# Kernel tuning notes

Hardware: AMD Instinct MI355X
Metric: run time of the kernel (lower is better)

Reference implementation:

```python
import jax, jax.numpy as jnp
import numpy as np

POOL = 7; SR = 2; SCALE = 1.0 / 16
NUM_CLASSES = 21
NMS_THR = 0.5; MIN_SIZE = 1.0; TOPK = 100; SCORE_THR = 0.05
BBOX_CLIP = float(np.log(1000.0 / 16))


def roi_align(feat, rois):
    # feat: [C,H,W]; rois: [P,4] xyxy in image coords. torchvision aligned=True, sampling_ratio=2.
    C, H, W = feat.shape
    S = POOL * SR
    x0r = rois[:, 0] * SCALE - 0.5
    y0r = rois[:, 1] * SCALE - 0.5
    bw = (rois[:, 2] - rois[:, 0]) * SCALE / POOL
    bh = (rois[:, 3] - rois[:, 1]) * SCALE / POOL
    t = (jnp.arange(S, dtype=feat.dtype) + 0.5) / SR  # sample offsets in bin units
    ys = y0r[:, None] + bh[:, None] * t  # [P,S]
    xs = x0r[:, None] + bw[:, None] * t  # [P,S]
    vy = (ys >= -1.0) & (ys <= H)
    vx = (xs >= -1.0) & (xs <= W)
    y = jnp.clip(ys, 0.0, H - 1)
    x = jnp.clip(xs, 0.0, W - 1)
    yl = jnp.floor(y).astype(jnp.int32); xl = jnp.floor(x).astype(jnp.int32)
    yh = jnp.minimum(yl + 1, H - 1);     xh = jnp.minimum(xl + 1, W - 1)
    ly = y - yl; lx = x - xl
    hy = 1.0 - ly; hx = 1.0 - lx

    def g(Yi, Xi):  # -> [C,P,S,S]
        return feat[:, Yi[:, :, None], Xi[:, None, :]]

    val = (g(yl, xl) * (hy[:, :, None] * hx[:, None, :])
         + g(yl, xh) * (hy[:, :, None] * lx[:, None, :])
         + g(yh, xl) * (ly[:, :, None] * hx[:, None, :])
         + g(yh, xh) * (ly[:, :, None] * lx[:, None, :]))
    val = val * (vy[:, :, None] & vx[:, None, :])[None].astype(feat.dtype)
    P = rois.shape[0]
    val = val.reshape(C, P, POOL, SR, POOL, SR).mean(axis=(3, 5))  # avg over 2x2 samples/bin
    return val.transpose(1, 0, 2, 3)  # [P,C,POOL,POOL]


def decode(pred, proposals):
    # pred: [N,K,4] (dx,dy,dw,dh); proposals: [N,4]
    w = proposals[:, 2] - proposals[:, 0]
    h = proposals[:, 3] - proposals[:, 1]
    cx = proposals[:, 0] + 0.5 * w
    cy = proposals[:, 1] + 0.5 * h
    dx, dy = pred[..., 0], pred[..., 1]
    dw = jnp.minimum(pred[..., 2], BBOX_CLIP)
    dh = jnp.minimum(pred[..., 3], BBOX_CLIP)
    pcx = dx * w[:, None] + cx[:, None]
    pcy = dy * h[:, None] + cy[:, None]
    pw = jnp.exp(dw) * w[:, None]
    ph = jnp.exp(dh) * h[:, None]
    return jnp.stack([pcx - 0.5 * pw, pcy - 0.5 * ph, pcx + 0.5 * pw, pcy + 0.5 * ph], axis=-1)


def box_iou(b):
    x1, y1, x2, y2 = b[:, 0], b[:, 1], b[:, 2], b[:, 3]
    area = (x2 - x1) * (y2 - y1)
    iw = jnp.maximum(jnp.minimum(x2[:, None], x2[None, :]) - jnp.maximum(x1[:, None], x1[None, :]), 0.0)
    ih = jnp.maximum(jnp.minimum(y2[:, None], y2[None, :]) - jnp.maximum(y1[:, None], y1[None, :]), 0.0)
    inter = iw * ih
    return inter / (area[:, None] + area[None, :] - inter)


def filter_predictions(boxes, labels, scores):
    # score threshold + min-size + per-class greedy NMS + topK, static shapes (padded to TOPK)
    N = scores.shape[0]
    ws = boxes[:, 2] - boxes[:, 0]
    hs = boxes[:, 3] - boxes[:, 1]
    valid = (scores > SCORE_THR) & (ws >= MIN_SIZE) & (hs >= MIN_SIZE)
    skey = jnp.where(valid, scores, -jnp.inf)
    order = jnp.argsort(-skey)
    b = boxes[order]; s = skey[order]; l = labels[order]; v = valid[order]
    # batched_nms via per-class coordinate offset
    off = jax.lax.stop_gradient(jnp.max(boxes) + 1.0)
    ob = jax.lax.stop_gradient(b) + (l.astype(b.dtype) * off)[:, None]
    iou = box_iou(ob)  # [N,N]
    idx = jnp.arange(N)

    def body(keep, i):
        sup = (iou[i] > NMS_THR) & keep[i] & (idx > i)
        return keep & ~sup, None

    keep, _ = jax.lax.scan(body, v, idx)
    rank = jnp.cumsum(keep) - 1
    final = keep & (rank < TOPK)
    pick = jnp.argsort(jnp.where(final, idx, N))[:TOPK]  # kept indices in score order, padded
    ok = final[pick]
    out_boxes = jnp.where(ok[:, None], b[pick], 0.0)
    out_scores = jnp.where(ok, s[pick], 0.0)
    out_labels = jnp.where(ok, l[pick], -1)
    return out_boxes, out_labels, out_scores


def roi_head_forward(image, feat, proposals, fc6_w, fc6_b, fc7_w, fc7_b, cls_w, cls_b, reg_w, reg_b):
    H_img, W_img = image.shape[-2], image.shape[-1]
    pooled = roi_align(feat[0], proposals)  # [P,C,7,7]
    x = pooled.reshape(pooled.shape[0], -1)
    x = jax.nn.relu(x @ fc6_w.T + fc6_b)
    x = jax.nn.relu(x @ fc7_w.T + fc7_b)
    cls_scores = x @ cls_w.T + cls_b                       # [P,K]
    box_pred = (x @ reg_w.T + reg_b).reshape(-1, NUM_CLASSES, 4)
    boxes = decode(box_pred, proposals)                    # [P,K,4]
    scores = jax.nn.softmax(cls_scores, axis=-1)
    boxes = jnp.stack([boxes[..., 0].clip(0, W_img), boxes[..., 1].clip(0, H_img),
                       boxes[..., 2].clip(0, W_img), boxes[..., 3].clip(0, H_img)], axis=-1)
    labels = jnp.broadcast_to(jnp.arange(NUM_CLASSES), scores.shape)
    boxes = boxes[:, 1:].reshape(-1, 4)
    scores = scores[:, 1:].reshape(-1)
    labels = (labels[:, 1:] - 1).reshape(-1)
    return filter_predictions(boxes, labels, scores)


def setup_inputs() -> dict:
    key = jax.random.key(0)
    ks = jax.random.split(key, 12)
    H_img, W_img = 800, 1072
    P, C = 300, 512
    image = jnp.zeros((1, 3, H_img, W_img), jnp.float32)
    feat = jax.random.normal(ks[0], (1, C, H_img // 16, W_img // 16), jnp.float32)
    cx = jax.random.uniform(ks[1], (P,)) * W_img
    cy = jax.random.uniform(ks[2], (P,)) * H_img
    bw = 20.0 + jax.random.uniform(ks[3], (P,)) * 300.0
    bh = 20.0 + jax.random.uniform(ks[4], (P,)) * 300.0
    proposals = jnp.stack([jnp.clip(cx - bw / 2, 0, W_img), jnp.clip(cy - bh / 2, 0, H_img),
                           jnp.clip(cx + bw / 2, 0, W_img), jnp.clip(cy + bh / 2, 0, H_img)], axis=1)
    fin = C * POOL * POOL  # 25088
    D = 1024
    fc6_w = jax.random.normal(ks[5], (D, fin), jnp.float32) / np.sqrt(fin)
    fc6_b = jnp.zeros((D,), jnp.float32)
    fc7_w = jax.random.normal(ks[6], (D, D), jnp.float32) / np.sqrt(D)
    fc7_b = jnp.zeros((D,), jnp.float32)
    cls_w = jax.random.normal(ks[7], (NUM_CLASSES, D), jnp.float32) / np.sqrt(D)
    cls_b = jnp.zeros((NUM_CLASSES,), jnp.float32)
    reg_w = jax.random.normal(ks[8], (NUM_CLASSES * 4, D), jnp.float32) * 0.001
    reg_b = jnp.zeros((NUM_CLASSES * 4,), jnp.float32)
    return {"image": image, "feat": feat, "proposals": proposals,
            "fc6_w": fc6_w, "fc6_b": fc6_b, "fc7_w": fc7_w, "fc7_b": fc7_b,
            "cls_w": cls_w, "cls_b": cls_b, "reg_w": reg_w, "reg_b": reg_b}


def reference(image, feat, proposals, fc6_w, fc6_b, fc7_w, fc7_b, cls_w, cls_b, reg_w, reg_b):
    return roi_head_forward(image, feat, proposals, fc6_w, fc6_b, fc7_w, fc7_b, cls_w, cls_b, reg_w, reg_b)
```

## Files before the change

### kernel.cpp

```cpp
#include <hip/hip_runtime.h>
#include <hip/hip_bf16.h>
#include <math.h>

#define P_N   300
#define C_N   512
#define H_F   50
#define W_F   67
#define HW_F  3350
#define D_N   1024
#define FIN   25088
#define NCLS  21
#define NCAND 6000
#define W_IMG 1072.0f
#define H_IMG 800.0f
#define BBOX_CLIP_F 4.135166556742356f
#define KS6   42
#define STEPS6_PER_Z 19
#define KS7   16
#define STEPS7_PER_Z 2
#define KSH   16
#define STEPSH_PER_Z 2
#define NHEAD 128
#define NW    96
#define A_SCALE 16.0f
#define B_SCALE 256.0f
#define O_SCALE (1.0f / 4096.0f)

typedef __attribute__((ext_vector_type(8)))  _Float16 half8;
typedef __attribute__((ext_vector_type(16))) float    f32x16;

__device__ __forceinline__ void splitA(float f, _Float16& h, _Float16& l) {
  float fs = f * A_SCALE;
  h = (_Float16)fs;
  l = (_Float16)(fs - (float)h);
}

__global__ __launch_bounds__(256) void transpose_feat(const float* __restrict__ feat,
                                                      float* __restrict__ ft) {
  __shared__ float tile[32][33];
  const int s0 = blockIdx.x * 32, c0 = blockIdx.y * 32;
  const int tx = threadIdx.x, ty = threadIdx.y;
  for (int r = ty; r < 32; r += 8) {
    int c = c0 + r, s = s0 + tx;
    tile[r][tx] = (s < HW_F) ? feat[(size_t)c * HW_F + s] : 0.0f;
  }
  __syncthreads();
  for (int r = ty; r < 32; r += 8) {
    int s = s0 + r, c = c0 + tx;
    if (s < HW_F) ft[(size_t)s * C_N + c] = tile[tx][r];
  }
}

__global__ __launch_bounds__(256) void roi_align_k(const float* __restrict__ ft,
                                                   const float* __restrict__ rois,
                                                   _Float16* __restrict__ Xhi,
                                                   _Float16* __restrict__ Xlo) {
  __shared__ _Float16 hbuf[12544] __attribute__((aligned(16)));
  __shared__ _Float16 lbuf[12544] __attribute__((aligned(16)));
  __shared__ int   g_yl[14], g_yh[14], g_xl[14], g_xh[14];
  __shared__ float g_ly[14], g_hy[14], g_lx[14], g_hx[14];
  __shared__ int   g_vy[14], g_vx[14];

  const int p   = blockIdx.x;
  const int ch  = blockIdx.y;
  const int tid = threadIdx.x;

  if (tid < 14) {
    const float rx0 = rois[p*4+0], ry0 = rois[p*4+1], rx1 = rois[p*4+2], ry1 = rois[p*4+3];
    const float x0r = rx0 * 0.0625f - 0.5f;
    const float y0r = ry0 * 0.0625f - 0.5f;
    const float bw  = (rx1 - rx0) * 0.0625f * (1.0f / 7.0f);
    const float bh  = (ry1 - ry0) * 0.0625f * (1.0f / 7.0f);
    const float t   = ((float)tid + 0.5f) * 0.5f;

    const float ys = y0r + bh * t;
    g_vy[tid] = (ys >= -1.0f) && (ys <= (float)H_F);
    float y = fminf(fmaxf(ys, 0.0f), (float)(H_F - 1));
    int yi = (int)floorf(y);
    g_yl[tid] = yi; g_yh[tid] = min(yi + 1, H_F - 1);
    g_ly[tid] = y - (float)yi; g_hy[tid] = 1.0f - (y - (float)yi);

    const float xs = x0r + bw * t;
    g_vx[tid] = (xs >= -1.0f) && (xs <= (float)W_F);
    float x = fminf(fmaxf(xs, 0.0f), (float)(W_F - 1));
    int xi = (int)floorf(x);
    g_xl[tid] = xi; g_xh[tid] = min(xi + 1, W_F - 1);
    g_lx[tid] = x - (float)xi; g_hx[tid] = 1.0f - (x - (float)xi);
  }
  __syncthreads();

  const int c = ch * 256 + tid;
  for (int cell = 0; cell < 49; ++cell) {
    const int py = cell / 7;
    const int px = cell - py * 7;
    float acc = 0.0f;
#pragma unroll
    for (int sy = 0; sy < 2; ++sy) {
      const int iy = 2 * py + sy;
      if (!g_vy[iy]) continue;
      const float ly = g_ly[iy], hy = g_hy[iy];
      const int ry0i = g_yl[iy] * W_F, ry1i = g_yh[iy] * W_F;
#pragma unroll
      for (int sx = 0; sx < 2; ++sx) {
        const int ix = 2 * px + sx;
        if (!g_vx[ix]) continue;
        const float lx = g_lx[ix], hx = g_hx[ix];
        const float* b00 = ft + (size_t)(ry0i + g_xl[ix]) * C_N;
        const float* b01 = ft + (size_t)(ry0i + g_xh[ix]) * C_N;
        const float* b10 = ft + (size_t)(ry1i + g_xl[ix]) * C_N;
        const float* b11 = ft + (size_t)(ry1i + g_xh[ix]) * C_N;
        acc += (hy*hx)*b00[c] + (hy*lx)*b01[c] + (ly*hx)*b10[c] + (ly*lx)*b11[c];
      }
    }
    _Float16 h, l;
    splitA(acc * 0.25f, h, l);
    hbuf[tid * 49 + cell] = h;
    lbuf[tid * 49 + cell] = l;
  }
  __syncthreads();

  const size_t base = (size_t)p * FIN + (size_t)ch * 12544;
  const uint4* hs = (const uint4*)hbuf;
  const uint4* ls = (const uint4*)lbuf;
  uint4* dh = (uint4*)(Xhi + base);
  uint4* dl = (uint4*)(Xlo + base);
  for (int k = tid; k < 1568; k += 256) { dh[k] = hs[k]; dl[k] = ls[k]; }
}

__device__ __forceinline__ int swz(int slot, int ks) {
  return slot ^ ((slot >> 5) & 1) ^ (((slot >> 3) & 1) << 1) ^ ((ks & 1) << 2);
}

__global__ __launch_bounds__(256, 3) void gemm_f16_3p(
    const _Float16* __restrict__ Ahi, const _Float16* __restrict__ Alo,
    const float* __restrict__ Wt, float* __restrict__ Pt,
    int M, int K, int steps_per_z, int ldc)
{
  __shared__ _Float16 lds[16384];
  const int tid  = threadIdx.x;
  const int lane = tid & 63, wave = tid >> 6;
  const int wm = wave >> 1, wn = wave & 1;

  const int GX = gridDim.x, GY = gridDim.y;
  const int T  = GX * GY * gridDim.z;
  int flat = blockIdx.x + GX * (blockIdx.y + GY * blockIdx.z);
  if ((T & 7) == 0) flat = (flat & 7) * (T >> 3) + (flat >> 3);
  const int bx = flat % GX;
  const int by = (flat / GX) % GY;
  const int bz = flat / (GX * GY);

  const int m0 = bx * 128, n0 = by * 128;
  const int steps_total = K >> 5;
  const int s0 = bz * steps_per_z;
  const int s1 = min(s0 + steps_per_z, steps_total);

  f32x16 acc[2][2];
#pragma unroll
  for (int a = 0; a < 2; ++a)
#pragma unroll
    for (int b = 0; b < 2; ++b)
#pragma unroll
      for (int r = 0; r < 16; ++r) acc[a][b][r] = 0.f;

  const int srow = tid >> 2;
  const int j8   = tid & 3;
  const int ksW  = j8 >> 1, kc8 = j8 & 1;
  const int wslot = swz((kc8 << 5) | (srow & 31), ksW);

  for (int step = s0; step < s1; ++step) {
    const int kb = step << 5;
#pragma unroll
    for (int half = 0; half < 2; ++half) {
      const int row = srow + half * 64;
      const int mf  = row >> 5;
      const int gm  = m0 + row;
      uint4 vh = make_uint4(0,0,0,0), vl = make_uint4(0,0,0,0);
      if (gm < M) {
        vh = *reinterpret_cast<const uint4*>(Ahi + (size_t)gm * K + kb + j8 * 8);
        vl = *reinterpret_cast<const uint4*>(Alo + (size_t)gm * K + kb + j8 * 8);
      }
      const int base = (mf * 2 + ksW) * 512 + wslot * 8;
      *reinterpret_cast<uint4*>(&lds[base])        = vh;
      *reinterpret_cast<uint4*>(&lds[4096 + base]) = vl;
    }
#pragma unroll
    for (int half = 0; half < 2; ++half) {
      const int n = srow + half * 64;
      const float* wp = Wt + (size_t)(n0 + n) * K + kb + j8 * 8;
      const float4 f0 = *reinterpret_cast<const float4*>(wp);
      const float4 f1 = *reinterpret_cast<const float4*>(wp + 4);
      float fv[8] = {f0.x, f0.y, f0.z, f0.w, f1.x, f1.y, f1.z, f1.w};
      union { _Float16 h[8]; uint4 v; } uh, ul;
#pragma unroll
      for (int e = 0; e < 8; ++e) {
        float fs = fv[e] * B_SCALE;
        uh.h[e] = (_Float16)fs;
        ul.h[e] = (_Float16)(fs - (float)uh.h[e]);
      }
      const int nf = n >> 5;
      const int base = 8192 + (nf * 2 + ksW) * 512 + wslot * 8;
      *reinterpret_cast<uint4*>(&lds[base])        = uh.v;
      *reinterpret_cast<uint4*>(&lds[4096 + base]) = ul.v;
    }
    __syncthreads();
#pragma unroll
    for (int ks = 0; ks < 2; ++ks) {
      const int rslot = swz(lane, ks) * 8;
      half8 ah[2], al[2], bh[2], bl[2];
#pragma unroll
      for (int mi = 0; mi < 2; ++mi) {
        const int mf = wm * 2 + mi;
        ah[mi] = *reinterpret_cast<const half8*>(&lds[(mf * 2 + ks) * 512 + rslot]);
        al[mi] = *reinterpret_cast<const half8*>(&lds[4096 + (mf * 2 + ks) * 512 + rslot]);
      }
#pragma unroll
      for (int ni = 0; ni < 2; ++ni) {
        const int nf = wn * 2 + ni;
        bh[ni] = *reinterpret_cast<const half8*>(&lds[8192  + (nf * 2 + ks) * 512 + rslot]);
        bl[ni] = *reinterpret_cast<const half8*>(&lds[12288 + (nf * 2 + ks) * 512 + rslot]);
      }
#pragma unroll
      for (int mi = 0; mi < 2; ++mi)
#pragma unroll
        for (int ni = 0; ni < 2; ++ni) {
          acc[mi][ni] = __builtin_amdgcn_mfma_f32_32x32x16_f16(ah[mi], bh[ni], acc[mi][ni], 0, 0, 0);
          acc[mi][ni] = __builtin_amdgcn_mfma_f32_32x32x16_f16(ah[mi], bl[ni], acc[mi][ni], 0, 0, 0);
          acc[mi][ni] = __builtin_amdgcn_mfma_f32_32x32x16_f16(al[mi], bh[ni], acc[mi][ni], 0, 0, 0);
        }
    }
    __syncthreads();
  }
  const int col = lane & 31, rhi = lane >> 5;
  float* outp = Pt + (size_t)bz * ((size_t)M * ldc);
#pragma unroll
  for (int mi = 0; mi < 2; ++mi)
#pragma unroll
    for (int ni = 0; ni < 2; ++ni) {
      const int n = n0 + (wn * 2 + ni) * 32 + col;
      if (n >= ldc) continue;
#pragma unroll
      for (int r = 0; r < 16; ++r) {
        const int m = m0 + (wm * 2 + mi) * 32 + ((r & 3) + 8 * (r >> 2) + 4 * rhi);
        if (m < M) outp[(size_t)m * ldc + n] = acc[mi][ni][r] * O_SCALE;
      }
    }
}

__global__ __launch_bounds__(256) void reduce_bias(
    const float* __restrict__ Pt, const float* __restrict__ bias,
    float* __restrict__ out_f32, _Float16* __restrict__ out_hi, _Float16* __restrict__ out_lo,
    int MN, int KS, int nmask, int relu)
{
  int i = blockIdx.x * 256 + threadIdx.x;
  if (i >= MN) return;
  float s = 0.0f;
  for (int k = 0; k < KS; ++k) s += Pt[(size_t)k * MN + i];
  s += bias[i & nmask];
  if (relu) s = fmaxf(s, 0.0f);
  if (out_f32) out_f32[i] = s;
  if (out_hi) {
    _Float16 h, l; splitA(s, h, l);
    out_hi[i] = h; out_lo[i] = l;
  }
}

__global__ __launch_bounds__(256) void prep_head(const float* __restrict__ cls_w,
                                                 const float* __restrict__ cls_b,
                                                 const float* __restrict__ reg_w,
                                                 const float* __restrict__ reg_b,
                                                 float* __restrict__ Wpad,
                                                 float* __restrict__ bpad,
                                                 int* __restrict__ vcount) {
  const int row = blockIdx.x;
  const int t = threadIdx.x;
  if (row == 0 && t == 0) *vcount = 0;
  const float* src = (row < NCLS) ? (cls_w + (size_t)row * D_N)
                   : (row < 105)  ? (reg_w + (size_t)(row - NCLS) * D_N) : nullptr;
  float4 v = make_float4(0.f, 0.f, 0.f, 0.f);
  if (src) v = reinterpret_cast<const float4*>(src)[t];
  reinterpret_cast<float4*>(Wpad + (size_t)row * D_N)[t] = v;
  if (t == 0)
    bpad[row] = (row < NCLS) ? cls_b[row] : (row < 105) ? reg_b[row - NCLS] : 0.0f;
}

__global__ __launch_bounds__(64) void decode_kernel(const float* __restrict__ logits,
                                                    const float* __restrict__ props,
                                                    float* __restrict__ cboxes,
                                                    unsigned long long* __restrict__ ckeys,
                                                    int* __restrict__ vcount) {
  const int p = blockIdx.x;
  const int lane = threadIdx.x;
  const float* lg = logits + (size_t)p * NHEAD;

  float s = (lane < NCLS) ? lg[lane] : -__builtin_inff();
  float mx = s;
#pragma unroll
  for (int off = 32; off > 0; off >>= 1) mx = fmaxf(mx, __shfl_xor(mx, off));
  float e = (lane < NCLS) ? expf(s - mx) : 0.0f;
  float sum = e;
#pragma unroll
  for (int off = 32; off > 0; off >>= 1) sum += __shfl_xor(sum, off);
  const float sm = e / sum;

  if (lane >= 1 && lane < NCLS) {
    const int c = lane;
    const float x0 = props[p*4+0], y0 = props[p*4+1], x1 = props[p*4+2], y1 = props[p*4+3];
    const float w = x1 - x0, hh = y1 - y0;
    const float cx = x0 + 0.5f * w, cy = y0 + 0.5f * hh;
    const float dx = lg[NCLS + c*4 + 0];
    const float dy = lg[NCLS + c*4 + 1];
    const float dw = fminf(lg[NCLS + c*4 + 2], BBOX_CLIP_F);
    const float dh = fminf(lg[NCLS + c*4 + 3], BBOX_CLIP_F);
    const float pcx = dx * w + cx, pcy = dy * hh + cy;
    const float pw = expf(dw) * w, ph = expf(dh) * hh;
    float bx0 = pcx - 0.5f * pw, by0 = pcy - 0.5f * ph;
    float bx1 = pcx + 0.5f * pw, by1 = pcy + 0.5f * ph;
    bx0 = fminf(fmaxf(bx0, 0.0f), W_IMG);
    by0 = fminf(fmaxf(by0, 0.0f), H_IMG);
    bx1 = fminf(fmaxf(bx1, 0.0f), W_IMG);
    by1 = fminf(fmaxf(by1, 0.0f), H_IMG);
    const int idx = p * 20 + (c - 1);
    cboxes[idx*4+0] = bx0; cboxes[idx*4+1] = by0;
    cboxes[idx*4+2] = bx1; cboxes[idx*4+3] = by1;
    const bool valid = (sm > 0.05f) && ((bx1 - bx0) >= 1.0f) && ((by1 - by0) >= 1.0f);
    if (valid) {
      int pos = atomicAdd(vcount, 1);
      unsigned u = __float_as_uint(sm);
      ckeys[pos] = ((unsigned long long)(~u) << 32) | (unsigned)idx;
    }
  }
}

__global__ __launch_bounds__(1024) void sort_gather(const unsigned long long* __restrict__ ckeys,
                                                    const int* __restrict__ vcount,
                                                    const float* __restrict__ cboxes,
                                                    float4* __restrict__ sbox,
                                                    float* __restrict__ sscore,
                                                    int* __restrict__ slab) {
  __shared__ unsigned long long keys[8192];
  const int tid = threadIdx.x;
  const int V = *vcount;
  int Npad = 64; while (Npad < V) Npad <<= 1;
  for (int i = tid; i < Npad; i += 1024)
    keys[i] = (i < V) ? ckeys[i] : ~0ULL;
  __syncthreads();
  for (int kk = 2; kk <= Npad; kk <<= 1) {
    for (int j = kk >> 1; j > 0; j >>= 1) {
      for (int i = tid; i < Npad; i += 1024) {
        int ij = i ^ j;
        if (ij > i) {
          unsigned long long a = keys[i], b = keys[ij];
          bool up = ((i & kk) == 0);
          if ((a > b) == up) { keys[i] = b; keys[ij] = a; }
        }
      }
      __syncthreads();
    }
  }
  for (int i = tid; i < V; i += 1024) {
    unsigned long long key = keys[i];
    int idx = (int)(key & 0xffffffffu);
    sbox[i]   = *reinterpret_cast<const float4*>(&cboxes[(size_t)idx * 4]);
    sscore[i] = __uint_as_float(~(unsigned)(key >> 32));
    slab[i]   = idx % 20;
  }
}

__global__ __launch_bounds__(256) void iou_matrix(const float4* __restrict__ sbox,
                                                  const int* __restrict__ slab,
                                                  const int* __restrict__ vcount,
                                                  unsigned long long* __restrict__ mask) {
  const int V = *vcount;
  const int i = blockIdx.x * 4 + (threadIdx.x >> 6);
  const int lane = threadIdx.x & 63;
  if (i >= V) return;
  const float4 bi = sbox[i];
  const int li = slab[i];
  const float ai = (bi.z - bi.x) * (bi.w - bi.y);
  const int nw = (V + 63) >> 6;
  for (int w = 0; w < nw; ++w) {
    const int j = (w << 6) + lane;
    bool sup = false;
    if (j > i && j < V && slab[j] == li) {
      const float4 bj = sbox[j];
      const float iw = fminf(bi.z, bj.z) - fmaxf(bi.x, bj.x);
      const float ih = fminf(bi.w, bj.w) - fmaxf(bi.y, bj.y);
      const float inter = fmaxf(iw, 0.0f) * fmaxf(ih, 0.0f);
      const float aj = (bj.z - bj.x) * (bj.w - bj.y);
      sup = inter / (ai + aj - inter) > 0.5f;
    }
    const unsigned long long m = __ballot(sup);
    if (lane == 0) mask[(size_t)i * NW + w] = m;
  }
}

__device__ __forceinline__ unsigned long long bcast_live(unsigned long long live0,
                                                         unsigned long long live1, int w) {
  union { unsigned long long u; uint2 v; } t;
  t.u = (w < 64) ? live0 : live1;
  const int src = w & 63;
  const unsigned lo = __shfl(t.v.x, src);
  const unsigned hi = __shfl(t.v.y, src);
  return ((unsigned long long)hi << 32) | lo;
}

__global__ __launch_bounds__(64) void nms_scan(const float4* __restrict__ sbox,
                                               const float* __restrict__ sscore,
                                               const int* __restrict__ slab,
                                               const int* __restrict__ vcount,
                                               const unsigned long long* __restrict__ mask,
                                               float* __restrict__ out) {
  const int lane = threadIdx.x;
  const int V = min(*vcount, NCAND);
  const int nw = (V + 63) >> 6;
  unsigned long long live0 = ~0ULL, live1 = ~0ULL;
  int nk = 0;
  for (int w = 0; w < nw && nk < 100; ++w) {
    const int nb = V - (w << 6);
    const unsigned long long vmask = (nb >= 64) ? ~0ULL : ((1ULL << nb) - 1ULL);
    unsigned long long wv = bcast_live(live0, live1, w) & vmask;
    while (wv && nk < 100) {
      const int b = __ffsll((long long)wv) - 1;
      const int i = (w << 6) + b;
      if (lane == 0) {
        const float4 bb = sbox[i];
        out[nk*4+0] = bb.x; out[nk*4+1] = bb.y; out[nk*4+2] = bb.z; out[nk*4+3] = bb.w;
        out[400 + nk] = (float)slab[i];
        out[500 + nk] = sscore[i];
      }
      const unsigned long long* mrow = mask + (size_t)i * NW;
      if (lane < nw) live0 &= ~mrow[lane];
      if (64 + lane < nw) live1 &= ~mrow[64 + lane];
      nk++;
      wv = bcast_live(live0, live1, w) & vmask;
      wv &= (b == 63) ? 0ULL : ~((2ULL << b) - 1ULL);
    }
  }
  for (int r = nk + lane; r < 100; r += 64) {
    out[r*4+0] = 0.0f; out[r*4+1] = 0.0f; out[r*4+2] = 0.0f; out[r*4+3] = 0.0f;
    out[400 + r] = -1.0f;
    out[500 + r] = 0.0f;
  }
}

extern "C" void kernel_launch(void* const* d_in, const int* in_sizes, int n_in,
                              void* d_out, int out_size, void* d_ws, size_t ws_size,
                              hipStream_t stream) {
  const float* feat   = (const float*)d_in[1];
  const float* props  = (const float*)d_in[2];
  const float* fc6_w  = (const float*)d_in[3];
  const float* fc6_b  = (const float*)d_in[4];
  const float* fc7_w  = (const float*)d_in[5];
  const float* fc7_b  = (const float*)d_in[6];
  const float* cls_w  = (const float*)d_in[7];
  const float* cls_b  = (const float*)d_in[8];
  const float* reg_w  = (const float*)d_in[9];
  const float* reg_b  = (const float*)d_in[10];

  char* ws = (char*)d_ws;
  size_t off = 0;
  auto alloc = [&](size_t bytes) -> void* {
    void* p = ws + off;
    off += (bytes + 255) & ~(size_t)255;
    return p;
  };

  _Float16* Xhi  = (_Float16*)alloc((size_t)P_N * FIN * 2);
  _Float16* Xlo  = (_Float16*)alloc((size_t)P_N * FIN * 2);
  float*    Pt   = (float*)alloc((size_t)KS6 * P_N * D_N * 4);
  _Float16* h6hi = (_Float16*)alloc((size_t)P_N * D_N * 2);
  _Float16* h6lo = (_Float16*)alloc((size_t)P_N * D_N * 2);
  _Float16* h7hi = (_Float16*)alloc((size_t)P_N * D_N * 2);
  _Float16* h7lo = (_Float16*)alloc((size_t)P_N * D_N * 2);
  float*    Wpad = (float*)alloc((size_t)NHEAD * D_N * 4);
  float*    bpad = (float*)alloc((size_t)NHEAD * 4);
  float*  logits = (float*)alloc((size_t)P_N * NHEAD * 4);
  float*  cboxes = (float*)alloc((size_t)NCAND * 4 * 4);
  unsigned long long* ckeys = (unsigned long long*)alloc((size_t)NCAND * 8);
  float4*   sbox = (float4*)alloc((size_t)NCAND * 16);
  float*  sscore = (float*)alloc((size_t)NCAND * 4);
  int*      slab = (int*)alloc((size_t)NCAND * 4);
  unsigned long long* supmask = (unsigned long long*)alloc((size_t)NCAND * NW * 8);
  int*    vcount = (int*)alloc(256);
  float* ft = Pt;
  (void)ws_size; (void)in_sizes; (void)n_in; (void)out_size;

  prep_head<<<NHEAD, 256, 0, stream>>>(cls_w, cls_b, reg_w, reg_b, Wpad, bpad, vcount);
  transpose_feat<<<dim3((HW_F + 31) / 32, C_N / 32), dim3(32, 8), 0, stream>>>(feat, ft);
  roi_align_k<<<dim3(P_N, 2), 256, 0, stream>>>(ft, props, Xhi, Xlo);
  gemm_f16_3p<<<dim3(3, 8, KS6), 256, 0, stream>>>(Xhi, Xlo, fc6_w, Pt, P_N, FIN, STEPS6_PER_Z, D_N);
  reduce_bias<<<(P_N * D_N + 255) / 256, 256, 0, stream>>>(
      Pt, fc6_b, nullptr, h6hi, h6lo, P_N * D_N, KS6, D_N - 1, 1);
  gemm_f16_3p<<<dim3(3, 8, KS7), 256, 0, stream>>>(h6hi, h6lo, fc7_w, Pt, P_N, D_N, STEPS7_PER_Z, D_N);
  reduce_bias<<<(P_N * D_N + 255) / 256, 256, 0, stream>>>(
      Pt, fc7_b, nullptr, h7hi, h7lo, P_N * D_N, KS7, D_N - 1, 1);
  gemm_f16_3p<<<dim3(3, 1, KSH), 256, 0, stream>>>(h7hi, h7lo, Wpad, Pt, P_N, D_N, STEPSH_PER_Z, NHEAD);
  reduce_bias<<<(P_N * NHEAD + 255) / 256, 256, 0, stream>>>(
      Pt, bpad, logits, nullptr, nullptr, P_N * NHEAD, KSH, NHEAD - 1, 0);
  decode_kernel<<<P_N, 64, 0, stream>>>(logits, props, cboxes, ckeys, vcount);
  sort_gather<<<1, 1024, 0, stream>>>(ckeys, vcount, cboxes, sbox, sscore, slab);
  iou_matrix<<<(NCAND + 3) / 4, 256, 0, stream>>>(sbox, slab, vcount, supmask);
  nms_scan<<<1, 64, 0, stream>>>(sbox, sscore, slab, vcount, supmask, (float*)d_out);
}
```

Baseline: 343.2 us.

## Register-prefetch next K tile in GEMM, halve fc6 split-K, merge prep kernels

The GEMM main loop now loads the next K-step's A and W tiles into registers before writing the current tile to LDS and computing on it. This overlaps global load latency with the MFMA work. The fc6 split-K factor drops from 42 to 21, which doubles steps per block and halves the partial-sum traffic, but also halves the grid. The head-weight padding kernel is folded into the feature transpose kernel to save one launch. The prefetch costs extra registers, which could hurt occupancy at 3 blocks per CU.

```diff
diff --git a/kernel.cpp b/kernel.cpp
--- a/kernel.cpp
+++ b/kernel.cpp
@@ -14,8 +14,8 @@
 #define W_IMG 1072.0f
 #define H_IMG 800.0f
 #define BBOX_CLIP_F 4.135166556742356f
-#define KS6   42
-#define STEPS6_PER_Z 19
+#define KS6   21
+#define STEPS6_PER_Z 38
 #define KS7   16
 #define STEPS7_PER_Z 2
 #define KSH   16
@@ -25,6 +25,7 @@
 #define A_SCALE 16.0f
 #define B_SCALE 256.0f
 #define O_SCALE (1.0f / 4096.0f)
+#define TBLK  1680
 
 typedef __attribute__((ext_vector_type(8)))  _Float16 half8;
 typedef __attribute__((ext_vector_type(16))) float    f32x16;
@@ -35,19 +36,41 @@
   l = (_Float16)(fs - (float)h);
 }
 
-__global__ __launch_bounds__(256) void transpose_feat(const float* __restrict__ feat,
-                                                      float* __restrict__ ft) {
+__global__ __launch_bounds__(256) void prep_transpose(const float* __restrict__ feat,
+                                                      float* __restrict__ ft,
+                                                      const float* __restrict__ cls_w,
+                                                      const float* __restrict__ cls_b,
+                                                      const float* __restrict__ reg_w,
+                                                      const float* __restrict__ reg_b,
+                                                      float* __restrict__ Wpad,
+                                                      float* __restrict__ bpad,
+                                                      int* __restrict__ vcount) {
   __shared__ float tile[32][33];
-  const int s0 = blockIdx.x * 32, c0 = blockIdx.y * 32;
-  const int tx = threadIdx.x, ty = threadIdx.y;
-  for (int r = ty; r < 32; r += 8) {
-    int c = c0 + r, s = s0 + tx;
-    tile[r][tx] = (s < HW_F) ? feat[(size_t)c * HW_F + s] : 0.0f;
-  }
-  __syncthreads();
-  for (int r = ty; r < 32; r += 8) {
-    int s = s0 + r, c = c0 + tx;
-    if (s < HW_F) ft[(size_t)s * C_N + c] = tile[tx][r];
+  const int bid = blockIdx.x;
+  const int tid = threadIdx.x;
+  if (bid < TBLK) {
+    const int bx = bid % 105, byy = bid / 105;
+    const int s0 = bx * 32, c0 = byy * 32;
+    const int tx = tid & 31, ty = tid >> 5;
+    for (int r = ty; r < 32; r += 8) {
+      int c = c0 + r, s = s0 + tx;
+      tile[r][tx] = (s < HW_F) ? feat[(size_t)c * HW_F + s] : 0.0f;
+    }
+    __syncthreads();
+    for (int r = ty; r < 32; r += 8) {
+      int s = s0 + r, c = c0 + tx;
+      if (s < HW_F) ft[(size_t)s * C_N + c] = tile[tx][r];
+    }
+  } else {
+    const int row = bid - TBLK;
+    if (row == 0 && tid == 0) *vcount = 0;
+    const float* src = (row < NCLS) ? (cls_w + (size_t)row * D_N)
+                     : (row < 105)  ? (reg_w + (size_t)(row - NCLS) * D_N) : nullptr;
+    float4 v = make_float4(0.f, 0.f, 0.f, 0.f);
+    if (src) v = reinterpret_cast<const float4*>(src)[tid];
+    reinterpret_cast<float4*>(Wpad + (size_t)row * D_N)[tid] = v;
+    if (tid == 0)
+      bpad[row] = (row < NCLS) ? cls_b[row] : (row < 105) ? reg_b[row - NCLS] : 0.0f;
   }
 }
 
@@ -131,6 +154,58 @@
   return slot ^ ((slot >> 5) & 1) ^ (((slot >> 3) & 1) << 1) ^ ((ks & 1) << 2);
 }
 
+struct SReg { uint4 ah0, ah1, al0, al1; float4 b00, b01, b10, b11; };
+
+__device__ __forceinline__ void stage_load(SReg& R, const _Float16* __restrict__ Ahi,
+                                           const _Float16* __restrict__ Alo,
+                                           const float* __restrict__ Wt,
+                                           int M, int K, int m0, int n0,
+                                           int srow, int j8, int kb) {
+  const int gm0 = m0 + srow, gm1 = m0 + srow + 64;
+  R.ah0 = make_uint4(0,0,0,0); R.al0 = R.ah0; R.ah1 = R.ah0; R.al1 = R.ah0;
+  if (gm0 < M) {
+    R.ah0 = *reinterpret_cast<const uint4*>(Ahi + (size_t)gm0 * K + kb + j8 * 8);
+    R.al0 = *reinterpret_cast<const uint4*>(Alo + (size_t)gm0 * K + kb + j8 * 8);
+  }
+  if (gm1 < M) {
+    R.ah1 = *reinterpret_cast<const uint4*>(Ahi + (size_t)gm1 * K + kb + j8 * 8);
+    R.al1 = *reinterpret_cast<const uint4*>(Alo + (size_t)gm1 * K + kb + j8 * 8);
+  }
+  const float* wp0 = Wt + (size_t)(n0 + srow) * K + kb + j8 * 8;
+  const float* wp1 = Wt + (size_t)(n0 + srow + 64) * K + kb + j8 * 8;
+  R.b00 = *reinterpret_cast<const float4*>(wp0);
+  R.b01 = *reinterpret_cast<const float4*>(wp0 + 4);
+  R.b10 = *reinterpret_cast<const float4*>(wp1);
+  R.b11 = *reinterpret_cast<const float4*>(wp1 + 4);
+}
+
+__device__ __forceinline__ void stage_write(const SReg& R, _Float16* lds,
+                                            int srow, int ksW, int wslot) {
+  const int mf0 = srow >> 5, mf1 = (srow + 64) >> 5;
+  const int base0 = (mf0 * 2 + ksW) * 512 + wslot * 8;
+  const int base1 = (mf1 * 2 + ksW) * 512 + wslot * 8;
+  *reinterpret_cast<uint4*>(&lds[base0])        = R.ah0;
+  *reinterpret_cast<uint4*>(&lds[4096 + base0]) = R.al0;
+  *reinterpret_cast<uint4*>(&lds[base1])        = R.ah1;
+  *reinterpret_cast<uint4*>(&lds[4096 + base1]) = R.al1;
+  float fv0[8] = {R.b00.x, R.b00.y, R.b00.z, R.b00.w, R.b01.x, R.b01.y, R.b01.z, R.b01.w};
+  float fv1[8] = {R.b10.x, R.b10.y, R.b10.z, R.b10.w, R.b11.x, R.b11.y, R.b11.z, R.b11.w};
+  union { _Float16 h[8]; uint4 v; } uh0, ul0, uh1, ul1;
+#pragma unroll
+  for (int e = 0; e < 8; ++e) {
+    float fs0 = fv0[e] * B_SCALE;
+    uh0.h[e] = (_Float16)fs0;
+    ul0.h[e] = (_Float16)(fs0 - (float)uh0.h[e]);
+    float fs1 = fv1[e] * B_SCALE;
+    uh1.h[e] = (_Float16)fs1;
+    ul1.h[e] = (_Float16)(fs1 - (float)uh1.h[e]);
+  }
+  *reinterpret_cast<uint4*>(&lds[8192  + base0]) = uh0.v;
+  *reinterpret_cast<uint4*>(&lds[12288 + base0]) = ul0.v;
+  *reinterpret_cast<uint4*>(&lds[8192  + base1]) = uh1.v;
+  *reinterpret_cast<uint4*>(&lds[12288 + base1]) = ul1.v;
+}
+
 __global__ __launch_bounds__(256, 3) void gemm_f16_3p(
     const _Float16* __restrict__ Ahi, const _Float16* __restrict__ Alo,
     const float* __restrict__ Wt, float* __restrict__ Pt,
@@ -167,42 +242,7 @@
   const int ksW  = j8 >> 1, kc8 = j8 & 1;
   const int wslot = swz((kc8 << 5) | (srow & 31), ksW);
 
-  for (int step = s0; step < s1; ++step) {
-    const int kb = step << 5;
-#pragma unroll
-    for (int half = 0; half < 2; ++half) {
-      const int row = srow + half * 64;
-      const int mf  = row >> 5;
-      const int gm  = m0 + row;
-      uint4 vh = make_uint4(0,0,0,0), vl = make_uint4(0,0,0,0);
-      if (gm < M) {
-        vh = *reinterpret_cast<const uint4*>(Ahi + (size_t)gm * K + kb + j8 * 8);
-        vl = *reinterpret_cast<const uint4*>(Alo + (size_t)gm * K + kb + j8 * 8);
-      }
-      const int base = (mf * 2 + ksW) * 512 + wslot * 8;
-      *reinterpret_cast<uint4*>(&lds[base])        = vh;
-      *reinterpret_cast<uint4*>(&lds[4096 + base]) = vl;
-    }
-#pragma unroll
-    for (int half = 0; half < 2; ++half) {
-      const int n = srow + half * 64;
-      const float* wp = Wt + (size_t)(n0 + n) * K + kb + j8 * 8;
-      const float4 f0 = *reinterpret_cast<const float4*>(wp);
-      const float4 f1 = *reinterpret_cast<const float4*>(wp + 4);
-      float fv[8] = {f0.x, f0.y, f0.z, f0.w, f1.x, f1.y, f1.z, f1.w};
-      union { _Float16 h[8]; uint4 v; } uh, ul;
-#pragma unroll
-      for (int e = 0; e < 8; ++e) {
-        float fs = fv[e] * B_SCALE;
-        uh.h[e] = (_Float16)fs;
-        ul.h[e] = (_Float16)(fs - (float)uh.h[e]);
-      }
-      const int nf = n >> 5;
-      const int base = 8192 + (nf * 2 + ksW) * 512 + wslot * 8;
-      *reinterpret_cast<uint4*>(&lds[base])        = uh.v;
-      *reinterpret_cast<uint4*>(&lds[4096 + base]) = ul.v;
-    }
-    __syncthreads();
+  auto compute = [&]() {
 #pragma unroll
     for (int ks = 0; ks < 2; ++ks) {
       const int rslot = swz(lane, ks) * 8;
@@ -228,8 +268,25 @@
           acc[mi][ni] = __builtin_amdgcn_mfma_f32_32x32x16_f16(al[mi], bh[ni], acc[mi][ni], 0, 0, 0);
         }
     }
+  };
+
+  SReg R0, R1;
+  if (s0 < s1) stage_load(R0, Ahi, Alo, Wt, M, K, m0, n0, srow, j8, s0 << 5);
+  for (int s = s0; s < s1; s += 2) {
+    if (s + 1 < s1) stage_load(R1, Ahi, Alo, Wt, M, K, m0, n0, srow, j8, (s + 1) << 5);
+    stage_write(R0, lds, srow, ksW, wslot);
     __syncthreads();
-  }
+    compute();
+    __syncthreads();
+    if (s + 1 < s1) {
+      if (s + 2 < s1) stage_load(R0, Ahi, Alo, Wt, M, K, m0, n0, srow, j8, (s + 2) << 5);
+      stage_write(R1, lds, srow, ksW, wslot);
+      __syncthreads();
+      compute();
+      __syncthreads();
+    }
+  }
+
   const int col = lane & 31, rhi = lane >> 5;
   float* outp = Pt + (size_t)bz * ((size_t)M * ldc);
 #pragma unroll
@@ -262,25 +319,6 @@
     _Float16 h, l; splitA(s, h, l);
     out_hi[i] = h; out_lo[i] = l;
   }
-}
-
-__global__ __launch_bounds__(256) void prep_head(const float* __restrict__ cls_w,
-                                                 const float* __restrict__ cls_b,
-                                                 const float* __restrict__ reg_w,
-                                                 const float* __restrict__ reg_b,
-                                                 float* __restrict__ Wpad,
-                                                 float* __restrict__ bpad,
-                                                 int* __restrict__ vcount) {
-  const int row = blockIdx.x;
-  const int t = threadIdx.x;
-  if (row == 0 && t == 0) *vcount = 0;
-  const float* src = (row < NCLS) ? (cls_w + (size_t)row * D_N)
-                   : (row < 105)  ? (reg_w + (size_t)(row - NCLS) * D_N) : nullptr;
-  float4 v = make_float4(0.f, 0.f, 0.f, 0.f);
-  if (src) v = reinterpret_cast<const float4*>(src)[t];
-  reinterpret_cast<float4*>(Wpad + (size_t)row * D_N)[t] = v;
-  if (t == 0)
-    bpad[row] = (row < NCLS) ? cls_b[row] : (row < 105) ? reg_b[row - NCLS] : 0.0f;
 }
 
 __global__ __launch_bounds__(64) void decode_kernel(const float* __restrict__ logits,
@@ -485,8 +523,8 @@
   float* ft = Pt;
   (void)ws_size; (void)in_sizes; (void)n_in; (void)out_size;
 
-  prep_head<<<NHEAD, 256, 0, stream>>>(cls_w, cls_b, reg_w, reg_b, Wpad, bpad, vcount);
-  transpose_feat<<<dim3((HW_F + 31) / 32, C_N / 32), dim3(32, 8), 0, stream>>>(feat, ft);
+  prep_transpose<<<TBLK + NHEAD, 256, 0, stream>>>(feat, ft, cls_w, cls_b, reg_w, reg_b,
+                                                   Wpad, bpad, vcount);
   roi_align_k<<<dim3(P_N, 2), 256, 0, stream>>>(ft, props, Xhi, Xlo);
   gemm_f16_3p<<<dim3(3, 8, KS6), 256, 0, stream>>>(Xhi, Xlo, fc6_w, Pt, P_N, FIN, STEPS6_PER_Z, D_N);
   reduce_bias<<<(P_N * D_N + 255) / 256, 256, 0, stream>>>(
```

New measurement: 379.7 us. 10.6% more time.

## Enlarge GEMM M-tile to 192 rows and fuse head-prep into transpose kernel

Applied to the files above, without the earlier changes.

Widens the GEMM block tile from 128 to 192 rows of M, so 300 proposals fit in 2 M-tiles instead of 3. This cuts padded-row waste and means each block loads the converted fp32 weights fewer times overall. fc6 split-K is also retuned from 42 to 40 slices of 20 steps. The separate head-weight padding kernel is merged into the feature transpose kernel to save a launch. In exchange the kernel uses more LDS and accumulator registers per block, which may lower occupancy at the declared bound of 3 blocks.

```diff
diff --git a/kernel.cpp b/kernel.cpp
--- a/kernel.cpp
+++ b/kernel.cpp
@@ -14,8 +14,8 @@
 #define W_IMG 1072.0f
 #define H_IMG 800.0f
 #define BBOX_CLIP_F 4.135166556742356f
-#define KS6   42
-#define STEPS6_PER_Z 19
+#define KS6   40
+#define STEPS6_PER_Z 20
 #define KS7   16
 #define STEPS7_PER_Z 2
 #define KSH   16
@@ -25,6 +25,7 @@
 #define A_SCALE 16.0f
 #define B_SCALE 256.0f
 #define O_SCALE (1.0f / 4096.0f)
+#define TBLK  1680
 
 typedef __attribute__((ext_vector_type(8)))  _Float16 half8;
 typedef __attribute__((ext_vector_type(16))) float    f32x16;
@@ -35,19 +36,41 @@
   l = (_Float16)(fs - (float)h);
 }
 
-__global__ __launch_bounds__(256) void transpose_feat(const float* __restrict__ feat,
-                                                      float* __restrict__ ft) {
+__global__ __launch_bounds__(256) void prep_transpose(const float* __restrict__ feat,
+                                                      float* __restrict__ ft,
+                                                      const float* __restrict__ cls_w,
+                                                      const float* __restrict__ cls_b,
+                                                      const float* __restrict__ reg_w,
+                                                      const float* __restrict__ reg_b,
+                                                      float* __restrict__ Wpad,
+                                                      float* __restrict__ bpad,
+                                                      int* __restrict__ vcount) {
   __shared__ float tile[32][33];
-  const int s0 = blockIdx.x * 32, c0 = blockIdx.y * 32;
-  const int tx = threadIdx.x, ty = threadIdx.y;
-  for (int r = ty; r < 32; r += 8) {
-    int c = c0 + r, s = s0 + tx;
-    tile[r][tx] = (s < HW_F) ? feat[(size_t)c * HW_F + s] : 0.0f;
-  }
-  __syncthreads();
-  for (int r = ty; r < 32; r += 8) {
-    int s = s0 + r, c = c0 + tx;
-    if (s < HW_F) ft[(size_t)s * C_N + c] = tile[tx][r];
+  const int bid = blockIdx.x;
+  const int tid = threadIdx.x;
+  if (bid < TBLK) {
+    const int bx = bid % 105, byy = bid / 105;
+    const int s0 = bx * 32, c0 = byy * 32;
+    const int tx = tid & 31, ty = tid >> 5;
+    for (int r = ty; r < 32; r += 8) {
+      int c = c0 + r, s = s0 + tx;
+      tile[r][tx] = (s < HW_F) ? feat[(size_t)c * HW_F + s] : 0.0f;
+    }
+    __syncthreads();
+    for (int r = ty; r < 32; r += 8) {
+      int s = s0 + r, c = c0 + tx;
+      if (s < HW_F) ft[(size_t)s * C_N + c] = tile[tx][r];
+    }
+  } else {
+    const int row = bid - TBLK;
+    if (row == 0 && tid == 0) *vcount = 0;
+    const float* src = (row < NCLS) ? (cls_w + (size_t)row * D_N)
+                     : (row < 105)  ? (reg_w + (size_t)(row - NCLS) * D_N) : nullptr;
+    float4 v = make_float4(0.f, 0.f, 0.f, 0.f);
+    if (src) v = reinterpret_cast<const float4*>(src)[tid];
+    reinterpret_cast<float4*>(Wpad + (size_t)row * D_N)[tid] = v;
+    if (tid == 0)
+      bpad[row] = (row < NCLS) ? cls_b[row] : (row < 105) ? reg_b[row - NCLS] : 0.0f;
   }
 }
 
@@ -136,7 +159,7 @@
     const float* __restrict__ Wt, float* __restrict__ Pt,
     int M, int K, int steps_per_z, int ldc)
 {
-  __shared__ _Float16 lds[16384];
+  __shared__ _Float16 lds[20480];
   const int tid  = threadIdx.x;
   const int lane = tid & 63, wave = tid >> 6;
   const int wm = wave >> 1, wn = wave & 1;
@@ -149,14 +172,14 @@
   const int by = (flat / GX) % GY;
   const int bz = flat / (GX * GY);
 
-  const int m0 = bx * 128, n0 = by * 128;
+  const int m0 = bx * 192, n0 = by * 128;
   const int steps_total = K >> 5;
   const int s0 = bz * steps_per_z;
   const int s1 = min(s0 + steps_per_z, steps_total);
 
-  f32x16 acc[2][2];
-#pragma unroll
-  for (int a = 0; a < 2; ++a)
+  f32x16 acc[3][2];
+#pragma unroll
+  for (int a = 0; a < 3; ++a)
 #pragma unroll
     for (int b = 0; b < 2; ++b)
 #pragma unroll
@@ -170,7 +193,7 @@
   for (int step = s0; step < s1; ++step) {
     const int kb = step << 5;
 #pragma unroll
-    for (int half = 0; half < 2; ++half) {
+    for (int half = 0; half < 3; ++half) {
       const int row = srow + half * 64;
       const int mf  = row >> 5;
       const int gm  = m0 + row;
@@ -181,7 +204,7 @@
       }
       const int base = (mf * 2 + ksW) * 512 + wslot * 8;
       *reinterpret_cast<uint4*>(&lds[base])        = vh;
-      *reinterpret_cast<uint4*>(&lds[4096 + base]) = vl;
+      *reinterpret_cast<uint4*>(&lds[6144 + base]) = vl;
     }
 #pragma unroll
     for (int half = 0; half < 2; ++half) {
@@ -198,7 +221,7 @@
         ul.h[e] = (_Float16)(fs - (float)uh.h[e]);
       }
       const int nf = n >> 5;
-      const int base = 8192 + (nf * 2 + ksW) * 512 + wslot * 8;
+      const int base = 12288 + (nf * 2 + ksW) * 512 + wslot * 8;
       *reinterpret_cast<uint4*>(&lds[base])        = uh.v;
       *reinterpret_cast<uint4*>(&lds[4096 + base]) = ul.v;
     }
@@ -206,21 +229,21 @@
 #pragma unroll
     for (int ks = 0; ks < 2; ++ks) {
       const int rslot = swz(lane, ks) * 8;
-      half8 ah[2], al[2], bh[2], bl[2];
-#pragma unroll
-      for (int mi = 0; mi < 2; ++mi) {
-        const int mf = wm * 2 + mi;
+      half8 ah[3], al[3], bh[2], bl[2];
+#pragma unroll
+      for (int mi = 0; mi < 3; ++mi) {
+        const int mf = wm * 3 + mi;
         ah[mi] = *reinterpret_cast<const half8*>(&lds[(mf * 2 + ks) * 512 + rslot]);
-        al[mi] = *reinterpret_cast<const half8*>(&lds[4096 + (mf * 2 + ks) * 512 + rslot]);
+        al[mi] = *reinterpret_cast<const half8*>(&lds[6144 + (mf * 2 + ks) * 512 + rslot]);
       }
 #pragma unroll
       for (int ni = 0; ni < 2; ++ni) {
         const int nf = wn * 2 + ni;
-        bh[ni] = *reinterpret_cast<const half8*>(&lds[8192  + (nf * 2 + ks) * 512 + rslot]);
-        bl[ni] = *reinterpret_cast<const half8*>(&lds[12288 + (nf * 2 + ks) * 512 + rslot]);
-      }
-#pragma unroll
-      for (int mi = 0; mi < 2; ++mi)
+        bh[ni] = *reinterpret_cast<const half8*>(&lds[12288 + (nf * 2 + ks) * 512 + rslot]);
+        bl[ni] = *reinterpret_cast<const half8*>(&lds[16384 + (nf * 2 + ks) * 512 + rslot]);
+      }
+#pragma unroll
+      for (int mi = 0; mi < 3; ++mi)
 #pragma unroll
         for (int ni = 0; ni < 2; ++ni) {
           acc[mi][ni] = __builtin_amdgcn_mfma_f32_32x32x16_f16(ah[mi], bh[ni], acc[mi][ni], 0, 0, 0);
@@ -233,14 +256,14 @@
   const int col = lane & 31, rhi = lane >> 5;
   float* outp = Pt + (size_t)bz * ((size_t)M * ldc);
 #pragma unroll
-  for (int mi = 0; mi < 2; ++mi)
+  for (int mi = 0; mi < 3; ++mi)
 #pragma unroll
     for (int ni = 0; ni < 2; ++ni) {
       const int n = n0 + (wn * 2 + ni) * 32 + col;
       if (n >= ldc) continue;
 #pragma unroll
       for (int r = 0; r < 16; ++r) {
-        const int m = m0 + (wm * 2 + mi) * 32 + ((r & 3) + 8 * (r >> 2) + 4 * rhi);
+        const int m = m0 + (wm * 3 + mi) * 32 + ((r & 3) + 8 * (r >> 2) + 4 * rhi);
         if (m < M) outp[(size_t)m * ldc + n] = acc[mi][ni][r] * O_SCALE;
       }
     }
@@ -262,25 +285,6 @@
     _Float16 h, l; splitA(s, h, l);
     out_hi[i] = h; out_lo[i] = l;
   }
-}
-
-__global__ __launch_bounds__(256) void prep_head(const float* __restrict__ cls_w,
-                                                 const float* __restrict__ cls_b,
-                                                 const float* __restrict__ reg_w,
-                                                 const float* __restrict__ reg_b,
-                                                 float* __restrict__ Wpad,
-                                                 float* __restrict__ bpad,
-                                                 int* __restrict__ vcount) {
-  const int row = blockIdx.x;
-  const int t = threadIdx.x;
-  if (row == 0 && t == 0) *vcount = 0;
-  const float* src = (row < NCLS) ? (cls_w + (size_t)row * D_N)
-                   : (row < 105)  ? (reg_w + (size_t)(row - NCLS) * D_N) : nullptr;
-  float4 v = make_float4(0.f, 0.f, 0.f, 0.f);
-  if (src) v = reinterpret_cast<const float4*>(src)[t];
-  reinterpret_cast<float4*>(Wpad + (size_t)row * D_N)[t] = v;
-  if (t == 0)
-    bpad[row] = (row < NCLS) ? cls_b[row] : (row < 105) ? reg_b[row - NCLS] : 0.0f;
 }
 
 __global__ __launch_bounds__(64) void decode_kernel(const float* __restrict__ logits,
@@ -485,16 +489,16 @@
   float* ft = Pt;
   (void)ws_size; (void)in_sizes; (void)n_in; (void)out_size;
 
-  prep_head<<<NHEAD, 256, 0, stream>>>(cls_w, cls_b, reg_w, reg_b, Wpad, bpad, vcount);
-  transpose_feat<<<dim3((HW_F + 31) / 32, C_N / 32), dim3(32, 8), 0, stream>>>(feat, ft);
+  prep_transpose<<<TBLK + NHEAD, 256, 0, stream>>>(feat, ft, cls_w, cls_b, reg_w, reg_b,
+                                                   Wpad, bpad, vcount);
   roi_align_k<<<dim3(P_N, 2), 256, 0, stream>>>(ft, props, Xhi, Xlo);
-  gemm_f16_3p<<<dim3(3, 8, KS6), 256, 0, stream>>>(Xhi, Xlo, fc6_w, Pt, P_N, FIN, STEPS6_PER_Z, D_N);
+  gemm_f16_3p<<<dim3(2, 8, KS6), 256, 0, stream>>>(Xhi, Xlo, fc6_w, Pt, P_N, FIN, STEPS6_PER_Z, D_N);
   reduce_bias<<<(P_N * D_N + 255) / 256, 256, 0, stream>>>(
       Pt, fc6_b, nullptr, h6hi, h6lo, P_N * D_N, KS6, D_N - 1, 1);
-  gemm_f16_3p<<<dim3(3, 8, KS7), 256, 0, stream>>>(h6hi, h6lo, fc7_w, Pt, P_N, D_N, STEPS7_PER_Z, D_N);
+  gemm_f16_3p<<<dim3(2, 8, KS7), 256, 0, stream>>>(h6hi, h6lo, fc7_w, Pt, P_N, D_N, STEPS7_PER_Z, D_N);
   reduce_bias<<<(P_N * D_N + 255) / 256, 256, 0, stream>>>(
       Pt, fc7_b, nullptr, h7hi, h7lo, P_N * D_N, KS7, D_N - 1, 1);
-  gemm_f16_3p<<<dim3(3, 1, KSH), 256, 0, stream>>>(h7hi, h7lo, Wpad, Pt, P_N, D_N, STEPSH_PER_Z, NHEAD);
+  gemm_f16_3p<<<dim3(2, 1, KSH), 256, 0, stream>>>(h7hi, h7lo, Wpad, Pt, P_N, D_N, STEPSH_PER_Z, NHEAD);
   reduce_bias<<<(P_N * NHEAD + 255) / 256, 256, 0, stream>>>(
       Pt, bpad, logits, nullptr, nullptr, P_N * NHEAD, KSH, NHEAD - 1, 0);
   decode_kernel<<<P_N, 64, 0, stream>>>(logits, props, cboxes, ckeys, vcount);
```

Result: no change. 343.9 us (+0.2%).
